# Kernel tuning notes

Measured on AMD Instinct MI355X. Metric: run time of the kernel, lower is better.

## Reference

```python
import jax, jax.numpy as jnp
import numpy as np

N_NODES = 100000
N_EDGES = 1600000
N_FEAT = 128
HIDN = 256
N_CLASSES = 47


def setup_inputs() -> dict:
    key = jax.random.key(0)
    ks = jax.random.split(key, 8)
    x = jax.random.normal(ks[0], (N_NODES, N_FEAT), dtype=jnp.float32)
    edge_index = jax.random.randint(ks[1], (2, N_EDGES), 0, N_NODES, dtype=jnp.int32)
    s1 = 1.0 / np.sqrt(N_FEAT)
    s2 = 1.0 / np.sqrt(HIDN)
    Wl1 = jax.random.normal(ks[2], (N_FEAT, HIDN), dtype=jnp.float32) * s1
    Wr1 = jax.random.normal(ks[3], (N_FEAT, HIDN), dtype=jnp.float32) * s1
    b1 = jnp.zeros((HIDN,), dtype=jnp.float32)
    Wl2 = jax.random.normal(ks[4], (HIDN, N_CLASSES), dtype=jnp.float32) * s2
    Wr2 = jax.random.normal(ks[5], (HIDN, N_CLASSES), dtype=jnp.float32) * s2
    b2 = jnp.zeros((N_CLASSES,), dtype=jnp.float32)
    return {"x": x, "edge_index": edge_index, "Wl1": Wl1, "Wr1": Wr1, "b1": b1,
            "Wl2": Wl2, "Wr2": Wr2, "b2": b2}


def _sage_conv(x, src, dst, Wl, Wr, b):
    # PyG SAGEConv (mean aggr): out = lin_l(mean_{j->i} x_j) + lin_r(x_i)
    n = x.shape[0]
    msg = x[src]                                                   # [E, F] gather
    agg = jax.ops.segment_sum(msg, dst, num_segments=n)            # [N, F]
    deg = jax.ops.segment_sum(jnp.ones((src.shape[0], 1), x.dtype), dst,
                              num_segments=n)                      # [N, 1]
    mean = agg / jnp.maximum(deg, 1.0)
    return mean @ Wl + b + x @ Wr


def reference(x, edge_index, Wl1, Wr1, b1, Wl2, Wr2, b2):
    src, dst = edge_index[0], edge_index[1]
    h = _sage_conv(x, src, dst, Wl1, Wr1, b1)
    h = jax.nn.relu(h)
    # dropout omitted (eval mode / deterministic baseline)
    out = _sage_conv(h, src, dst, Wl2, Wr2, b2)
    return out
```

## Files before the change

### kernel.cpp

```cpp
#include <hip/hip_runtime.h>

#define NN 100000
#define NE 1600000
#define NF 128
#define NH 256
#define NC 47
#define NB 391
#define CH 8192
#define NCH ((NE + CH - 1) / CH)

#define PB_HIST 0
#define PB_CAST (PB_HIST + NCH)
#define NCAST   (NN * NF / 4 / 256)
#define PB_BT1  (PB_CAST + NCAST)
#define PB_BT2  (PB_BT1 + 256)
#define PB_END  (PB_BT2 + 96)

typedef __attribute__((ext_vector_type(8))) short bf16x8;
typedef __attribute__((ext_vector_type(4))) float f32x4;
typedef __attribute__((ext_vector_type(2))) float f32x2;

typedef __attribute__((address_space(1))) const void as1_void;
typedef __attribute__((address_space(3))) void as3_void;
__device__ __forceinline__ void gload16(const void* g, void* l) {
    __builtin_amdgcn_global_load_lds((as1_void*)g, (as3_void*)l, 16, 0, 0);
}

__device__ inline unsigned short f2bf(float f) {
    unsigned u = __builtin_bit_cast(unsigned, f);
    unsigned r = u + 0x7fffu + ((u >> 16) & 1u);
    return (unsigned short)(r >> 16);
}
__device__ inline float bfl(unsigned u) {
    return __builtin_bit_cast(float, u << 16);
}


__global__ __launch_bounds__(256) void prep_k(const int* __restrict__ dst,
                                              int* __restrict__ chunk_hist,
                                              int* __restrict__ total,
                                              const float* __restrict__ x,
                                              unsigned short* __restrict__ xb,
                                              unsigned* __restrict__ xq,
                                              const float* __restrict__ Wl1,
                                              const float* __restrict__ Wr1,
                                              unsigned short* __restrict__ Bt1,
                                              const float* __restrict__ Wl2,
                                              const float* __restrict__ Wr2,
                                              unsigned short* __restrict__ Bt2) {
    __shared__ int h[NB];
    int tid = threadIdx.x;
    int blk = blockIdx.x;
    if (blk < PB_CAST) {
        int ch = blk;
        for (int i = tid; i < NB; i += 256) h[i] = 0;
        __syncthreads();
        int e0 = ch * CH;
        int e1 = min(e0 + CH, NE);
        for (int e = e0 + tid; e < e1; e += 256)
            atomicAdd(&h[dst[e] >> 8], 1);
        __syncthreads();
        for (int i = tid; i < NB; i += 256) {
            int v = h[i];
            chunk_hist[(size_t)ch * NB + i] = v;
            if (v) atomicAdd(&total[i], v);
        }
    } else if (blk < PB_BT1) {
        int i = (blk - PB_CAST) * 256 + tid;
        float4 v = *reinterpret_cast<const float4*>(x + (size_t)i * 4);
        ushort4 o;
        o.x = f2bf(v.x); o.y = f2bf(v.y); o.z = f2bf(v.z); o.w = f2bf(v.w);
        *reinterpret_cast<ushort4*>(xb + (size_t)i * 4) = o;
        int r = __builtin_amdgcn_cvt_pk_fp8_f32(v.x, v.y, 0, false);
        r = __builtin_amdgcn_cvt_pk_fp8_f32(v.z, v.w, r, true);
        xq[i] = (unsigned)r;
    } else if (blk < PB_BT2) {
        int idx = (blk - PB_BT1) * 256 + tid;
        int n = idx >> 8, k = idx & 255;
        float v = (k < 128) ? Wl1[(size_t)k * NH + n] : Wr1[(size_t)(k - 128) * NH + n];
        Bt1[idx] = f2bf(v);
    } else {
        int idx = (blk - PB_BT2) * 256 + tid;
        int n = idx >> 8, k = idx & 255;
        float v = 0.f;
        if (n < 47) v = Wl2[(size_t)k * NC + n];
        else if (n >= 48 && n < 95) v = Wr2[(size_t)k * NC + (n - 48)];
        Bt2[idx] = f2bf(v);
    }
}


__global__ __launch_bounds__(64) void scancol_k(const int* __restrict__ chunk_hist,
                                                const int* __restrict__ total,
                                                int* __restrict__ bucket_base,
                                                int* __restrict__ chunk_off) {
    int b = blockIdx.x;
    int lane = threadIdx.x;
    int base = 0;
    for (int i0 = 0; i0 < NB; i0 += 64) {
        int i = i0 + lane;
        base += (i < b) ? total[i] : 0;
    }
    #pragma unroll
    for (int off = 1; off < 64; off <<= 1)
        base += __shfl_xor(base, off);
    if (lane == 0) bucket_base[b] = base;
    int run = base;
    for (int c0 = 0; c0 < NCH; c0 += 64) {
        int c = c0 + lane;
        int v = (c < NCH) ? chunk_hist[(size_t)c * NB + b] : 0;
        int s = v;
        #pragma unroll
        for (int off = 1; off < 64; off <<= 1) {
            int t = __shfl_up(s, off);
            if (lane >= off) s += t;
        }
        if (c < NCH) chunk_off[(size_t)c * NB + b] = run + s - v;
        run += __shfl(s, 63);
    }
}

__global__ __launch_bounds__(256) void scatter2_k(const int* __restrict__ src,
                                                  const int* __restrict__ dst,
                                                  const int* __restrict__ chunk_off,
                                                  unsigned* __restrict__ ebuf) {
    __shared__ int cur[NB];
    int tid = threadIdx.x, ch = blockIdx.x;
    for (int i = tid; i < NB; i += 256)
        cur[i] = chunk_off[(size_t)ch * NB + i];
    __syncthreads();
    int e0 = ch * CH;
    int e1 = min(e0 + CH, NE);
    for (int e = e0 + tid; e < e1; e += 256) {
        int d = dst[e];
        int b = d >> 8;
        int p = atomicAdd(&cur[b], 1);
        ebuf[p] = ((unsigned)(d & 255) << 24) | (unsigned)src[e];
    }
}

__global__ __launch_bounds__(256) void build_csr_k(const unsigned* __restrict__ ebuf,
                                                   const int* __restrict__ bucket_base,
                                                   const int* __restrict__ bucket_cnt,
                                                   int* __restrict__ row_start,
                                                   int* __restrict__ deg,
                                                   float* __restrict__ inv_deg,
                                                   int* __restrict__ csr_src) {
    __shared__ int s[256];
    __shared__ int cursor[256];
    int tid = threadIdx.x;
    int b = blockIdx.x;
    int lo = b << 8;
    int ebase = bucket_base[b];
    int ne = bucket_cnt[b];

    s[tid] = 0;
    __syncthreads();
    for (int e = tid; e < ne; e += 256)
        atomicAdd(&s[ebuf[ebase + e] >> 24], 1);
    __syncthreads();
    int v = s[tid];
    __syncthreads();
    for (int off = 1; off < 256; off <<= 1) {
        int t = (tid >= off) ? s[tid - off] : 0;
        __syncthreads();
        s[tid] += t;
        __syncthreads();
    }
    int excl = s[tid] - v;
    int node = lo + tid;
    if (node < NN) {
        row_start[node] = ebase + excl;
        deg[node] = v;
        inv_deg[node] = 1.0f / (float)(v > 1 ? v : 1);
    }
    cursor[tid] = ebase + excl;
    __syncthreads();
    for (int e = tid; e < ne; e += 256) {
        unsigned u = ebuf[ebase + e];
        int p = atomicAdd(&cursor[u >> 24], 1);
        csr_src[p] = (int)(u & 0xFFFFFFu);
    }
}


__global__ __launch_bounds__(256) void agg_mean_128q_k(const unsigned* __restrict__ xq,
                                                       const int* __restrict__ csr_src,
                                                       const int* __restrict__ row_start,
                                                       const int* __restrict__ deg,
                                                       const float* __restrict__ inv_deg,
                                                       unsigned short* __restrict__ mean1) {
    int node = blockIdx.x * 16 + (threadIdx.x >> 4);
    int l16 = threadIdx.x & 15;
    if (node >= NN) return;
    int s0 = row_start[node];
    int d  = deg[node];
    f32x2 acc[4];
    #pragma unroll
    for (int k = 0; k < 4; ++k) acc[k] = f32x2{0.f, 0.f};
    int j = 0;
    for (; j + 3 < d; j += 4) {
        int sA = csr_src[s0 + j];
        int sB = csr_src[s0 + j + 1];
        int sC = csr_src[s0 + j + 2];
        int sD = csr_src[s0 + j + 3];
        uint2 wA = *reinterpret_cast<const uint2*>(xq + (size_t)sA * 32 + l16 * 2);
        uint2 wB = *reinterpret_cast<const uint2*>(xq + (size_t)sB * 32 + l16 * 2);
        uint2 wC = *reinterpret_cast<const uint2*>(xq + (size_t)sC * 32 + l16 * 2);
        uint2 wD = *reinterpret_cast<const uint2*>(xq + (size_t)sD * 32 + l16 * 2);
        acc[0] += __builtin_amdgcn_cvt_pk_f32_fp8((int)wA.x, false);
        acc[1] += __builtin_amdgcn_cvt_pk_f32_fp8((int)wA.x, true);
        acc[2] += __builtin_amdgcn_cvt_pk_f32_fp8((int)wA.y, false);
        acc[3] += __builtin_amdgcn_cvt_pk_f32_fp8((int)wA.y, true);
        acc[0] += __builtin_amdgcn_cvt_pk_f32_fp8((int)wB.x, false);
        acc[1] += __builtin_amdgcn_cvt_pk_f32_fp8((int)wB.x, true);
        acc[2] += __builtin_amdgcn_cvt_pk_f32_fp8((int)wB.y, false);
        acc[3] += __builtin_amdgcn_cvt_pk_f32_fp8((int)wB.y, true);
        acc[0] += __builtin_amdgcn_cvt_pk_f32_fp8((int)wC.x, false);
        acc[1] += __builtin_amdgcn_cvt_pk_f32_fp8((int)wC.x, true);
        acc[2] += __builtin_amdgcn_cvt_pk_f32_fp8((int)wC.y, false);
        acc[3] += __builtin_amdgcn_cvt_pk_f32_fp8((int)wC.y, true);
        acc[0] += __builtin_amdgcn_cvt_pk_f32_fp8((int)wD.x, false);
        acc[1] += __builtin_amdgcn_cvt_pk_f32_fp8((int)wD.x, true);
        acc[2] += __builtin_amdgcn_cvt_pk_f32_fp8((int)wD.y, false);
        acc[3] += __builtin_amdgcn_cvt_pk_f32_fp8((int)wD.y, true);
    }
    for (; j < d; ++j) {
        int s = csr_src[s0 + j];
        uint2 w = *reinterpret_cast<const uint2*>(xq + (size_t)s * 32 + l16 * 2);
        acc[0] += __builtin_amdgcn_cvt_pk_f32_fp8((int)w.x, false);
        acc[1] += __builtin_amdgcn_cvt_pk_f32_fp8((int)w.x, true);
        acc[2] += __builtin_amdgcn_cvt_pk_f32_fp8((int)w.y, false);
        acc[3] += __builtin_amdgcn_cvt_pk_f32_fp8((int)w.y, true);
    }
    float inv = inv_deg[node];
    bf16x8 o;
    #pragma unroll
    for (int k = 0; k < 4; ++k) {
        o[k * 2]     = (short)f2bf(acc[k].x * inv);
        o[k * 2 + 1] = (short)f2bf(acc[k].y * inv);
    }
    *reinterpret_cast<bf16x8*>(mean1 + (size_t)node * NF + l16 * 8) = o;
}

__global__ __launch_bounds__(256) void agg_mean_47q_add_k(const unsigned* __restrict__ tq,
                                                          const int* __restrict__ csr_src,
                                                          const int* __restrict__ row_start,
                                                          const int* __restrict__ deg,
                                                          const float* __restrict__ inv_deg,
                                                          float* __restrict__ out) {
    int node = blockIdx.x * 16 + (threadIdx.x >> 4);
    int l16 = threadIdx.x & 15;
    if (node >= NN) return;
    int s0 = row_start[node];
    int d  = deg[node];
    f32x2 a01 = {0.f, 0.f}, a23 = {0.f, 0.f};
    int j = 0;
    for (; j + 3 < d; j += 4) {
        int sA = csr_src[s0 + j];
        int sB = csr_src[s0 + j + 1];
        int sC = csr_src[s0 + j + 2];
        int sD = csr_src[s0 + j + 3];
        unsigned wA = tq[(size_t)sA * 16 + l16];
        unsigned wB = tq[(size_t)sB * 16 + l16];
        unsigned wC = tq[(size_t)sC * 16 + l16];
        unsigned wD = tq[(size_t)sD * 16 + l16];
        a01 += __builtin_amdgcn_cvt_pk_f32_fp8((int)wA, false);
        a23 += __builtin_amdgcn_cvt_pk_f32_fp8((int)wA, true);
        a01 += __builtin_amdgcn_cvt_pk_f32_fp8((int)wB, false);
        a23 += __builtin_amdgcn_cvt_pk_f32_fp8((int)wB, true);
        a01 += __builtin_amdgcn_cvt_pk_f32_fp8((int)wC, false);
        a23 += __builtin_amdgcn_cvt_pk_f32_fp8((int)wC, true);
        a01 += __builtin_amdgcn_cvt_pk_f32_fp8((int)wD, false);
        a23 += __builtin_amdgcn_cvt_pk_f32_fp8((int)wD, true);
    }
    for (; j < d; ++j) {
        int s = csr_src[s0 + j];
        unsigned w = tq[(size_t)s * 16 + l16];
        a01 += __builtin_amdgcn_cvt_pk_f32_fp8((int)w, false);
        a23 += __builtin_amdgcn_cvt_pk_f32_fp8((int)w, true);
    }
    float inv = inv_deg[node];
    int c0 = l16 * 4;
    float vals[4] = {a01.x, a01.y, a23.x, a23.y};
    #pragma unroll
    for (int m = 0; m < 4; ++m) {
        int col = c0 + m;
        if (col < NC) {
            size_t o = (size_t)node * NC + col;
            out[o] += vals[m] * inv;
        }
    }
}


__global__ __launch_bounds__(512) void gemm12_k(const unsigned short* __restrict__ mean1,
                                                const unsigned short* __restrict__ xb,
                                                const unsigned short* __restrict__ Bt1,
                                                const float* __restrict__ b1,
                                                const unsigned short* __restrict__ Bt2,
                                                const float* __restrict__ b2,
                                                unsigned char* __restrict__ tq,
                                                float* __restrict__ out) {
    __shared__ __align__(16) union SM {
        struct { short As[3][128 * 32]; short Bs[3][256 * 32]; } g;
        unsigned short Hs[128 * 256];
    } sm;
    const int tid = threadIdx.x;
    const int row0 = blockIdx.x * 128;
    const int lane = tid & 63;
    const int wid = tid >> 6;
    const int r15 = lane & 15;
    const int swz = ((lane >> 4) ^ ((lane >> 1) & 3)) & 3;

    const int wr = wid >> 2, wc = wid & 3;
    f32x4 acc[4][4];
    #pragma unroll
    for (int i = 0; i < 4; ++i)
        #pragma unroll
        for (int j = 0; j < 4; ++j)
            acc[i][j] = f32x4{0.f, 0.f, 0.f, 0.f};

    auto stage = [&](int buf, int kt) {
        {
            int row = tid >> 2, g = tid & 3;
            int grow = row0 + row;
            if (grow >= NN) grow = NN - 1;
            int gs = g ^ ((row >> 1) & 3);
            const unsigned short* asrc = (kt < 128) ? mean1 : xb;
            gload16(asrc + (size_t)grow * NF + (kt & 127) + gs * 8, &sm.g.As[buf][tid * 8]);
        }
        #pragma unroll
        for (int i = 0; i < 2; ++i) {
            int c = tid + i * 512;
            int rn = c >> 2, g = c & 3;
            int gs = g ^ ((rn >> 1) & 3);
            gload16(Bt1 + (size_t)rn * 256 + kt + gs * 8, &sm.g.Bs[buf][c * 8]);
        }
    };
    auto compute = [&](int buf) {
        bf16x8 a[4], b[4];
        #pragma unroll
        for (int mi = 0; mi < 4; ++mi)
            a[mi] = *reinterpret_cast<const bf16x8*>(&sm.g.As[buf][(wr * 64 + mi * 16 + r15) * 32 + swz * 8]);
        #pragma unroll
        for (int ni = 0; ni < 4; ++ni)
            b[ni] = *reinterpret_cast<const bf16x8*>(&sm.g.Bs[buf][(wc * 64 + ni * 16 + r15) * 32 + swz * 8]);
        #pragma unroll
        for (int mi = 0; mi < 4; ++mi)
            #pragma unroll
            for (int ni = 0; ni < 4; ++ni)
                acc[mi][ni] = __builtin_amdgcn_mfma_f32_16x16x32_bf16(a[mi], b[ni], acc[mi][ni], 0, 0, 0);
    };

    stage(0, 0);
    stage(1, 32);
    #pragma unroll 1
    for (int ks = 0; ks < 8; ++ks) {
        if (ks + 1 < 8) asm volatile("s_waitcnt vmcnt(3)" ::: "memory");
        else            asm volatile("s_waitcnt vmcnt(0)" ::: "memory");
        __builtin_amdgcn_s_barrier();
        if (ks + 2 < 8) stage((ks + 2) % 3, (ks + 2) * 32);
        compute(ks % 3);
    }
    __syncthreads();

    #pragma unroll
    for (int ni = 0; ni < 4; ++ni) {
        int col = wc * 64 + ni * 16 + r15;
        float bias = b1[col];
        int kgrp = col >> 3, within = col & 7;
        #pragma unroll
        for (int mi = 0; mi < 4; ++mi) {
            int rbase = wr * 64 + mi * 16 + (lane >> 4) * 4;
            f32x4 c = acc[mi][ni];
            #pragma unroll
            for (int q = 0; q < 4; ++q) {
                int row = rbase + q;
                float v = fmaxf(c[q] + bias, 0.f);
                sm.Hs[row * 256 + (kgrp ^ (row & 31)) * 8 + within] = f2bf(v);
            }
        }
    }
    __syncthreads();

    const int wr2 = wid >> 1, wc2 = wid & 1;
    f32x4 acc2[2][3];
    #pragma unroll
    for (int i = 0; i < 2; ++i)
        #pragma unroll
        for (int j = 0; j < 3; ++j)
            acc2[i][j] = f32x4{0.f, 0.f, 0.f, 0.f};

    #pragma unroll
    for (int kt = 0; kt < 256; kt += 32) {
        bf16x8 a2[2], b2f[3];
        #pragma unroll
        for (int mi = 0; mi < 2; ++mi) {
            int row = wr2 * 32 + mi * 16 + r15;
            int kgrp = (kt >> 3) + (lane >> 4);
            a2[mi] = *reinterpret_cast<const bf16x8*>(&sm.Hs[row * 256 + (kgrp ^ (row & 31)) * 8]);
        }
        #pragma unroll
        for (int ni = 0; ni < 3; ++ni) {
            int n = wc2 * 48 + ni * 16 + r15;
            b2f[ni] = *reinterpret_cast<const bf16x8*>(Bt2 + (size_t)n * 256 + kt + (lane >> 4) * 8);
        }
        #pragma unroll
        for (int mi = 0; mi < 2; ++mi)
            #pragma unroll
            for (int ni = 0; ni < 3; ++ni)
                acc2[mi][ni] = __builtin_amdgcn_mfma_f32_16x16x32_bf16(a2[mi], b2f[ni], acc2[mi][ni], 0, 0, 0);
    }

    #pragma unroll
    for (int ni = 0; ni < 3; ++ni) {
        int col = wc2 * 48 + ni * 16 + r15;
        float bias = (col >= 48 && col < 95) ? b2[col - 48] : 0.f;
        #pragma unroll
        for (int mi = 0; mi < 2; ++mi) {
            int rbase = row0 + wr2 * 32 + mi * 16 + (lane >> 4) * 4;
            f32x4 c = acc2[mi][ni];
            #pragma unroll
            for (int q = 0; q < 4; ++q) {
                int row = rbase + q;
                if (row < NN) {
                    if (col < 47) {
                        int p = __builtin_amdgcn_cvt_pk_fp8_f32(c[q], c[q], 0, false);
                        tq[(size_t)row * 64 + col] = (unsigned char)(p & 0xFF);
                    } else if (col >= 48 && col < 95) {
                        out[(size_t)row * NC + (col - 48)] = c[q] + bias;
                    }
                }
            }
        }
    }
}


extern "C" void kernel_launch(void* const* d_in, const int* in_sizes, int n_in,
                              void* d_out, int out_size, void* d_ws, size_t ws_size,
                              hipStream_t stream) {
    const float* x    = (const float*)d_in[0];
    const int*   eidx = (const int*)d_in[1];
    const float* Wl1  = (const float*)d_in[2];
    const float* Wr1  = (const float*)d_in[3];
    const float* b1   = (const float*)d_in[4];
    const float* Wl2  = (const float*)d_in[5];
    const float* Wr2  = (const float*)d_in[6];
    const float* b2   = (const float*)d_in[7];
    float* out = (float*)d_out;

    const int* src = eidx;
    const int* dst = eidx + NE;

    size_t off = 0;
    auto alloc = [&](size_t bytes) -> void* {
        void* p = (char*)d_ws + off;
        off += (bytes + 511) & ~(size_t)511;
        return p;
    };
    int*            deg        = (int*)alloc((size_t)NN * 4);
    int*            row_start  = (int*)alloc((size_t)NN * 4);
    float*          inv_deg    = (float*)alloc((size_t)NN * 4);
    int*            csr_src    = (int*)alloc((size_t)NE * 4);
    unsigned*       ebuf       = (unsigned*)alloc((size_t)NE * 4);
    int*            chunk_hist = (int*)alloc((size_t)NCH * NB * 4);
    int*            chunk_off  = (int*)alloc((size_t)NCH * NB * 4);
    int*            bkt_cnt    = (int*)alloc((size_t)NB * 4);
    int*            bkt_base   = (int*)alloc((size_t)NB * 4);
    unsigned short* xb         = (unsigned short*)alloc((size_t)NN * NF * 2);
    unsigned*       xq         = (unsigned*)alloc((size_t)NN * NF);
    unsigned short* mean1      = (unsigned short*)alloc((size_t)NN * NF * 2);
    unsigned char*  tq         = (unsigned char*)alloc((size_t)NN * 64);
    unsigned short* Bt1        = (unsigned short*)alloc((size_t)256 * 256 * 2);
    unsigned short* Bt2        = (unsigned short*)alloc((size_t)96 * 256 * 2);
    (void)ws_size; (void)n_in; (void)in_sizes; (void)out_size;

    hipMemsetAsync(bkt_cnt, 0, (size_t)NB * 4, stream);
    prep_k<<<PB_END, 256, 0, stream>>>(dst, chunk_hist, bkt_cnt,
                                       x, xb, xq, Wl1, Wr1, Bt1, Wl2, Wr2, Bt2);
    scancol_k<<<NB, 64, 0, stream>>>(chunk_hist, bkt_cnt, bkt_base, chunk_off);
    scatter2_k<<<NCH, 256, 0, stream>>>(src, dst, chunk_off, ebuf);
    build_csr_k<<<NB, 256, 0, stream>>>(ebuf, bkt_base, bkt_cnt,
                                        row_start, deg, inv_deg, csr_src);

    agg_mean_128q_k<<<(NN + 15) / 16, 256, 0, stream>>>(xq, csr_src, row_start, deg, inv_deg, mean1);

    gemm12_k<<<(NN + 127) / 128, 512, 0, stream>>>(mean1, xb, Bt1, b1, Bt2, b2, tq, out);

    agg_mean_47q_add_k<<<(NN + 15) / 16, 256, 0, stream>>>((const unsigned*)tq, csr_src, row_start, deg, inv_deg, out);
}
```

Before: 192.9 us.

## Load GEMM1 operands directly from global memory instead of staged LDS pipeline

Replaces the triple-buffered global_load_lds staging of A and B tiles in the first GEMM with direct per-lane vector loads from global memory into registers, removing the LDS union and barriers in the K loop. It also sets a minimum-occupancy launch bound so more blocks can be resident. The intent is to cut LDS traffic and synchronization and to raise occupancy. The trade-off is that each wave now reloads the B1 weights and A rows from cache without sharing through LDS, and the launch bound may cap registers.

```diff
diff --git a/kernel.cpp b/kernel.cpp
--- a/kernel.cpp
+++ b/kernel.cpp
@@ -19,12 +19,6 @@
 typedef __attribute__((ext_vector_type(8))) short bf16x8;
 typedef __attribute__((ext_vector_type(4))) float f32x4;
 typedef __attribute__((ext_vector_type(2))) float f32x2;
-
-typedef __attribute__((address_space(1))) const void as1_void;
-typedef __attribute__((address_space(3))) void as3_void;
-__device__ __forceinline__ void gload16(const void* g, void* l) {
-    __builtin_amdgcn_global_load_lds((as1_void*)g, (as3_void*)l, 16, 0, 0);
-}
 
 __device__ inline unsigned short f2bf(float f) {
     unsigned u = __builtin_bit_cast(unsigned, f);
@@ -294,24 +288,21 @@
 }
 
 
-__global__ __launch_bounds__(512) void gemm12_k(const unsigned short* __restrict__ mean1,
-                                                const unsigned short* __restrict__ xb,
-                                                const unsigned short* __restrict__ Bt1,
-                                                const float* __restrict__ b1,
-                                                const unsigned short* __restrict__ Bt2,
-                                                const float* __restrict__ b2,
-                                                unsigned char* __restrict__ tq,
-                                                float* __restrict__ out) {
-    __shared__ __align__(16) union SM {
-        struct { short As[3][128 * 32]; short Bs[3][256 * 32]; } g;
-        unsigned short Hs[128 * 256];
-    } sm;
+__global__ __launch_bounds__(512, 4) void gemm12_k(const unsigned short* __restrict__ mean1,
+                                                   const unsigned short* __restrict__ xb,
+                                                   const unsigned short* __restrict__ Bt1,
+                                                   const float* __restrict__ b1,
+                                                   const unsigned short* __restrict__ Bt2,
+                                                   const float* __restrict__ b2,
+                                                   unsigned char* __restrict__ tq,
+                                                   float* __restrict__ out) {
+    __shared__ __align__(16) unsigned short Hs[128 * 256];
     const int tid = threadIdx.x;
     const int row0 = blockIdx.x * 128;
     const int lane = tid & 63;
     const int wid = tid >> 6;
     const int r15 = lane & 15;
-    const int swz = ((lane >> 4) ^ ((lane >> 1) & 3)) & 3;
+    const int kg = lane >> 4;
 
     const int wr = wid >> 2, wc = wid & 3;
     f32x4 acc[4][4];
@@ -321,49 +312,33 @@
         for (int j = 0; j < 4; ++j)
             acc[i][j] = f32x4{0.f, 0.f, 0.f, 0.f};
 
-    auto stage = [&](int buf, int kt) {
-        {
-            int row = tid >> 2, g = tid & 3;
-            int grow = row0 + row;
-            if (grow >= NN) grow = NN - 1;
-            int gs = g ^ ((row >> 1) & 3);
-            const unsigned short* asrc = (kt < 128) ? mean1 : xb;
-            gload16(asrc + (size_t)grow * NF + (kt & 127) + gs * 8, &sm.g.As[buf][tid * 8]);
-        }
-        #pragma unroll
-        for (int i = 0; i < 2; ++i) {
-            int c = tid + i * 512;
-            int rn = c >> 2, g = c & 3;
-            int gs = g ^ ((rn >> 1) & 3);
-            gload16(Bt1 + (size_t)rn * 256 + kt + gs * 8, &sm.g.Bs[buf][c * 8]);
-        }
-    };
-    auto compute = [&](int buf) {
+    int arow[4];
+    #pragma unroll
+    for (int mi = 0; mi < 4; ++mi) {
+        int row = row0 + wr * 64 + mi * 16 + r15;
+        arow[mi] = (row < NN) ? row : (NN - 1);
+    }
+
+    #pragma unroll 2
+    for (int ks = 0; ks < 8; ++ks) {
+        int kt = ks * 32;
+        const unsigned short* asrc = (ks < 4) ? mean1 : xb;
+        int kb = (kt & 127) + kg * 8;
         bf16x8 a[4], b[4];
         #pragma unroll
         for (int mi = 0; mi < 4; ++mi)
-            a[mi] = *reinterpret_cast<const bf16x8*>(&sm.g.As[buf][(wr * 64 + mi * 16 + r15) * 32 + swz * 8]);
-        #pragma unroll
-        for (int ni = 0; ni < 4; ++ni)
-            b[ni] = *reinterpret_cast<const bf16x8*>(&sm.g.Bs[buf][(wc * 64 + ni * 16 + r15) * 32 + swz * 8]);
+            a[mi] = *reinterpret_cast<const bf16x8*>(asrc + (size_t)arow[mi] * NF + kb);
+        #pragma unroll
+        for (int ni = 0; ni < 4; ++ni) {
+            int n = wc * 64 + ni * 16 + r15;
+            b[ni] = *reinterpret_cast<const bf16x8*>(Bt1 + (size_t)n * 256 + kt + kg * 8);
+        }
         #pragma unroll
         for (int mi = 0; mi < 4; ++mi)
             #pragma unroll
             for (int ni = 0; ni < 4; ++ni)
                 acc[mi][ni] = __builtin_amdgcn_mfma_f32_16x16x32_bf16(a[mi], b[ni], acc[mi][ni], 0, 0, 0);
-    };
-
-    stage(0, 0);
-    stage(1, 32);
-    #pragma unroll 1
-    for (int ks = 0; ks < 8; ++ks) {
-        if (ks + 1 < 8) asm volatile("s_waitcnt vmcnt(3)" ::: "memory");
-        else            asm volatile("s_waitcnt vmcnt(0)" ::: "memory");
-        __builtin_amdgcn_s_barrier();
-        if (ks + 2 < 8) stage((ks + 2) % 3, (ks + 2) * 32);
-        compute(ks % 3);
-    }
-    __syncthreads();
+    }
 
     #pragma unroll
     for (int ni = 0; ni < 4; ++ni) {
@@ -378,7 +353,7 @@
             for (int q = 0; q < 4; ++q) {
                 int row = rbase + q;
                 float v = fmaxf(c[q] + bias, 0.f);
-                sm.Hs[row * 256 + (kgrp ^ (row & 31)) * 8 + within] = f2bf(v);
+                Hs[row * 256 + (kgrp ^ (row & 31)) * 8 + within] = f2bf(v);
             }
         }
     }
@@ -398,13 +373,13 @@
         #pragma unroll
         for (int mi = 0; mi < 2; ++mi) {
             int row = wr2 * 32 + mi * 16 + r15;
-            int kgrp = (kt >> 3) + (lane >> 4);
-            a2[mi] = *reinterpret_cast<const bf16x8*>(&sm.Hs[row * 256 + (kgrp ^ (row & 31)) * 8]);
+            int kgrp = (kt >> 3) + kg;
+            a2[mi] = *reinterpret_cast<const bf16x8*>(&Hs[row * 256 + (kgrp ^ (row & 31)) * 8]);
         }
         #pragma unroll
         for (int ni = 0; ni < 3; ++ni) {
             int n = wc2 * 48 + ni * 16 + r15;
-            b2f[ni] = *reinterpret_cast<const bf16x8*>(Bt2 + (size_t)n * 256 + kt + (lane >> 4) * 8);
+            b2f[ni] = *reinterpret_cast<const bf16x8*>(Bt2 + (size_t)n * 256 + kt + kg * 8);
         }
         #pragma unroll
         for (int mi = 0; mi < 2; ++mi)
```

After: 232.2 us. 20.4% more time.
